# Kernel tuning notes

Hardware: AMD Instinct MI355X
Metric: run time of the kernel (lower is better)

## Reference

```python
import jax, jax.numpy as jnp
import numpy as np

EMBED = 1024
HEADS = 16
HEAD_DIM = EMBED // HEADS
MLP_DIM = 4096
EPS = 1e-5


def setup_inputs() -> dict:
    key = jax.random.key(0)
    ks = jax.random.split(key, 12)
    s = lambda d: 1.0 / np.sqrt(d)
    return {
        "x": jax.random.normal(ks[0], (8, 1024, EMBED), dtype=jnp.float32),
        "ln1_g": jnp.ones((EMBED,), jnp.float32),
        "ln1_b": jnp.zeros((EMBED,), jnp.float32),
        "w_qkv": jax.random.normal(ks[1], (EMBED, 3 * EMBED), jnp.float32) * s(EMBED),
        "b_qkv": jnp.zeros((3 * EMBED,), jnp.float32),
        "w_proj": jax.random.normal(ks[2], (EMBED, EMBED), jnp.float32) * s(EMBED),
        "b_proj": jnp.zeros((EMBED,), jnp.float32),
        "ln2_g": jnp.ones((EMBED,), jnp.float32),
        "ln2_b": jnp.zeros((EMBED,), jnp.float32),
        "w_fc1": jax.random.normal(ks[3], (EMBED, MLP_DIM), jnp.float32) * s(EMBED),
        "b_fc1": jnp.zeros((MLP_DIM,), jnp.float32),
        "w_fc2": jax.random.normal(ks[4], (MLP_DIM, EMBED), jnp.float32) * s(MLP_DIM),
        "b_fc2": jnp.zeros((EMBED,), jnp.float32),
    }


def _layernorm(x, g, b):
    mu = jnp.mean(x, axis=-1, keepdims=True)
    var = jnp.mean(jnp.square(x - mu), axis=-1, keepdims=True)
    return (x - mu) * jax.lax.rsqrt(var + EPS) * g + b


def reference(x, ln1_g, ln1_b, w_qkv, b_qkv, w_proj, b_proj,
              ln2_g, ln2_b, w_fc1, b_fc1, w_fc2, b_fc2):
    B, N, D = x.shape
    scale = HEAD_DIM ** -0.5

    # --- attention branch ---
    h = _layernorm(x, ln1_g, ln1_b)
    qkv = h @ w_qkv + b_qkv                       # [B,N,3D]
    qkv = qkv.reshape(B, N, 3, HEADS, HEAD_DIM)
    q, k, v = jnp.moveaxis(qkv, 2, 0)             # each [B,N,H,hd]
    attn = jnp.einsum('bqhd,bkhd->bhqk', q, k) * scale
    attn = jax.nn.softmax(attn, axis=-1)
    out = jnp.einsum('bhqk,bkhd->bqhd', attn, v).reshape(B, N, D)
    x = x + (out @ w_proj + b_proj)

    # --- MLP branch ---
    h = _layernorm(x, ln2_g, ln2_b)
    h = jax.nn.gelu(h @ w_fc1 + b_fc1, approximate=False)
    x = x + (h @ w_fc2 + b_fc2)
    return x
```

## Files before the change

kernel.cpp:

```cpp
#include <hip/hip_runtime.h>
#include <cstdint>


typedef unsigned short u16;
typedef short short8 __attribute__((ext_vector_type(8)));
typedef float floatx4 __attribute__((ext_vector_type(4)));

#define GLB(p) ((const __attribute__((address_space(1))) void*)(p))
#define LDSP(p) ((__attribute__((address_space(3))) void*)(p))

__device__ __forceinline__ u16 f2bf(float f) {
    uint32_t u = __float_as_uint(f);
    u += 0x7fffu + ((u >> 16) & 1u);
    return (u16)(u >> 16);
}
__device__ __forceinline__ uint32_t pack2(float a, float b) {
    return (uint32_t)f2bf(a) | ((uint32_t)f2bf(b) << 16);
}
__device__ __forceinline__ float fast_gelu(float v) {
    float u = v * (0.7978845608f + 0.0356774081f * v * v);
    float e = __expf(2.0f * u);
    float th = 1.0f - 2.0f * __builtin_amdgcn_rcpf(e + 1.0f);
    return 0.5f * v * (1.0f + th);
}

__global__ __launch_bounds__(256) void transpose_cast_kernel(
    const float* __restrict__ W, u16* __restrict__ Wt, int K, int N)
{
    __shared__ float tile[32][33];
    int n0 = blockIdx.x * 32, k0 = blockIdx.y * 32;
    int tx = threadIdx.x, ty = threadIdx.y;
    #pragma unroll
    for (int i = 0; i < 4; ++i)
        tile[ty + i * 8][tx] = W[(size_t)(k0 + ty + i * 8) * N + n0 + tx];
    __syncthreads();
    #pragma unroll
    for (int i = 0; i < 4; ++i)
        Wt[(size_t)(n0 + ty + i * 8) * K + k0 + tx] = f2bf(tile[tx][ty + i * 8]);
}

__global__ __launch_bounds__(256) void ln_kernel(
    const float* __restrict__ x, const float* __restrict__ gw,
    const float* __restrict__ bw, u16* __restrict__ out)
{
    const int row = blockIdx.x, tid = threadIdx.x;
    float4 v = ((const float4*)(x + (size_t)row * 1024))[tid];
    float s  = v.x + v.y + v.z + v.w;
    float ss = v.x * v.x + v.y * v.y + v.z * v.z + v.w * v.w;
    #pragma unroll
    for (int off = 32; off > 0; off >>= 1) {
        s  += __shfl_down(s, off);
        ss += __shfl_down(ss, off);
    }
    __shared__ float red[8];
    if ((tid & 63) == 0) { red[tid >> 6] = s; red[4 + (tid >> 6)] = ss; }
    __syncthreads();
    float S  = red[0] + red[1] + red[2] + red[3];
    float SS = red[4] + red[5] + red[6] + red[7];
    float mu  = S * (1.0f / 1024.0f);
    float var = SS * (1.0f / 1024.0f) - mu * mu;
    float rs  = rsqrtf(var + 1e-5f);
    float4 g4 = ((const float4*)gw)[tid];
    float4 b4 = ((const float4*)bw)[tid];
    u16* o = out + (size_t)row * 1024 + tid * 4;
    o[0] = f2bf((v.x - mu) * rs * g4.x + b4.x);
    o[1] = f2bf((v.y - mu) * rs * g4.y + b4.y);
    o[2] = f2bf((v.z - mu) * rs * g4.z + b4.z);
    o[3] = f2bf((v.w - mu) * rs * g4.w + b4.w);
}

#define MODE_BF16      0
#define MODE_BF16_GELU 1
#define MODE_F32_RES   2
#define MODE_QKV       3

template<int MODE>
__global__ __launch_bounds__(256) void gemm_bt_kernel(
    const u16* __restrict__ A, const u16* __restrict__ Bt,
    const float* __restrict__ bias, const float* __restrict__ res,
    void* __restrict__ outv, u16* __restrict__ vt, int M, int N, int K)
{
    __shared__ __attribute__((aligned(16))) u16 As[128 * 64];
    __shared__ __attribute__((aligned(16))) u16 Bs[128 * 64];
    const int tid = threadIdx.x;
    const int wave = tid >> 6, lane = tid & 63;
    const int lg = lane >> 4, lc = lane & 15;
    const int m0 = blockIdx.y * 128, n0 = blockIdx.x * 128;
    const int wr = wave >> 1, wc = wave & 1;

    floatx4 acc[4][4];
    #pragma unroll
    for (int i = 0; i < 4; ++i)
        #pragma unroll
        for (int j = 0; j < 4; ++j) acc[i][j] = floatx4{0.f, 0.f, 0.f, 0.f};

    const int srow = lane >> 3;
    const int schunk = (lane & 7) ^ srow;
    const u16* Ag = A  + (size_t)(m0 + wave * 32 + srow) * K + schunk * 8;
    const u16* Bg = Bt + (size_t)(n0 + wave * 32 + srow) * K + schunk * 8;
    u16* Asw = &As[wave * 4 * 512];
    u16* Bsw = &Bs[wave * 4 * 512];

    const int kiters = K >> 6;
    for (int kt = 0; kt < kiters; ++kt) {
        #pragma unroll
        for (int j = 0; j < 4; ++j) {
            __builtin_amdgcn_global_load_lds(GLB(Ag + (size_t)j * 8 * K), LDSP(Asw + j * 512), 16, 0, 0);
            __builtin_amdgcn_global_load_lds(GLB(Bg + (size_t)j * 8 * K), LDSP(Bsw + j * 512), 16, 0, 0);
        }
        Ag += 64; Bg += 64;
        __syncthreads();
        #pragma unroll
        for (int ks = 0; ks < 2; ++ks) {
            short8 fa[4], fb[4];
            #pragma unroll
            for (int mt = 0; mt < 4; ++mt)
                fa[mt] = *(const short8*)&As[(wr * 64 + mt * 16 + lc) * 64 +
                                             (((ks * 4 + lg) ^ (lc & 7)) * 8)];
            #pragma unroll
            for (int nt = 0; nt < 4; ++nt)
                fb[nt] = *(const short8*)&Bs[(wc * 64 + nt * 16 + lc) * 64 +
                                             (((ks * 4 + lg) ^ (lc & 7)) * 8)];
            #pragma unroll
            for (int mt = 0; mt < 4; ++mt)
                #pragma unroll
                for (int nt = 0; nt < 4; ++nt)
                    acc[mt][nt] = __builtin_amdgcn_mfma_f32_16x16x32_bf16(fa[mt], fb[nt], acc[mt][nt], 0, 0, 0);
        }
        __syncthreads();
    }

    if (MODE == MODE_QKV && n0 >= 2048) {
        #pragma unroll
        for (int mt = 0; mt < 4; ++mt) {
            #pragma unroll
            for (int nt = 0; nt < 4; ++nt) {
                const int col = n0 + wc * 64 + nt * 16 + lc;
                const float bv = bias[col];
                const int hd = col - 2048;
                const int rowbase = m0 + wr * 64 + mt * 16 + lg * 4;
                const int b = rowbase >> 10, token = rowbase & 1023;
                float v0 = acc[mt][nt][0] + bv, v1 = acc[mt][nt][1] + bv;
                float v2 = acc[mt][nt][2] + bv, v3 = acc[mt][nt][3] + bv;
                uint2 pk = {pack2(v0, v1), pack2(v2, v3)};
                *(uint2*)&vt[((size_t)b * 1024 + hd) * 1024 + token] = pk;
            }
        }
        return;
    }
    #pragma unroll
    for (int mt = 0; mt < 4; ++mt) {
        #pragma unroll
        for (int nt = 0; nt < 4; ++nt) {
            const int col = n0 + wc * 64 + nt * 16 + lc;
            const float bv = bias[col];
            #pragma unroll
            for (int r = 0; r < 4; ++r) {
                const int row = m0 + wr * 64 + mt * 16 + lg * 4 + r;
                float v = acc[mt][nt][r] + bv;
                if (MODE == MODE_BF16 || MODE == MODE_QKV) {
                    ((u16*)outv)[(size_t)row * N + col] = f2bf(v);
                } else if (MODE == MODE_BF16_GELU) {
                    ((u16*)outv)[(size_t)row * N + col] = f2bf(fast_gelu(v));
                } else {
                    ((float*)outv)[(size_t)row * N + col] = v + res[(size_t)row * N + col];
                }
            }
        }
    }
}

__global__ __launch_bounds__(256) void attn_kernel(
    const u16* __restrict__ qkv, const u16* __restrict__ vtg, u16* __restrict__ out)
{
    const int bid = blockIdx.x;
    const int g = ((bid >> 7) << 3) | (bid & 7);
    const int qt = (bid >> 3) & 15;
    const int h = g & 15, b = g >> 4;
    const int tid = threadIdx.x, wave = tid >> 6, lane = tid & 63;
    const int lg = lane >> 4, lc = lane & 15;

    __shared__ __attribute__((aligned(16))) u16 Qs[64 * 64];
    __shared__ __attribute__((aligned(16))) u16 Ks[64 * 64];
    __shared__ __attribute__((aligned(16))) u16 Vts[64 * 64];
    __shared__ __attribute__((aligned(16))) u16 Ps[64 * 64];

    const int q0 = qt * 64;
    const size_t hb = ((size_t)b * 1024) * 3072 + h * 64;
    const u16* vhead = vtg + ((size_t)b * 1024 + h * 64) * 1024;
    const int srow = lane >> 3;
    const int schunk = (lane & 7) ^ srow;

    {
        const u16* Qg = qkv + hb + (size_t)(q0 + wave * 16 + srow) * 3072 + schunk * 8;
        u16* Qw = &Qs[wave * 1024];
        __builtin_amdgcn_global_load_lds(GLB(Qg), LDSP(Qw), 16, 0, 0);
        __builtin_amdgcn_global_load_lds(GLB(Qg + (size_t)8 * 3072), LDSP(Qw + 512), 16, 0, 0);
    }
    __syncthreads();
    short8 aq[2];
    aq[0] = *(const short8*)&Qs[(wave * 16 + lc) * 64 + (((0 + lg) ^ (lc & 7)) * 8)];
    aq[1] = *(const short8*)&Qs[(wave * 16 + lc) * 64 + (((4 + lg) ^ (lc & 7)) * 8)];

    floatx4 o[4];
    #pragma unroll
    for (int dt = 0; dt < 4; ++dt) o[dt] = floatx4{0.f, 0.f, 0.f, 0.f};
    float mprev = -INFINITY, lsum = 0.f;
    const float sc = 0.125f;

    for (int kt = 0; kt < 16; ++kt) {
        __syncthreads();
        {
            const u16* Kg = qkv + hb + 1024 +
                (size_t)(kt * 64 + wave * 16 + srow) * 3072 + schunk * 8;
            u16* Kw = &Ks[wave * 1024];
            __builtin_amdgcn_global_load_lds(GLB(Kg), LDSP(Kw), 16, 0, 0);
            __builtin_amdgcn_global_load_lds(GLB(Kg + (size_t)8 * 3072), LDSP(Kw + 512), 16, 0, 0);
        }
        {
            const u16* Vg = vhead + (size_t)(wave * 16 + srow) * 1024 + kt * 64 + schunk * 8;
            u16* Vw = &Vts[wave * 1024];
            __builtin_amdgcn_global_load_lds(GLB(Vg), LDSP(Vw), 16, 0, 0);
            __builtin_amdgcn_global_load_lds(GLB(Vg + (size_t)8 * 1024), LDSP(Vw + 512), 16, 0, 0);
        }
        __syncthreads();

        floatx4 st[4];
        #pragma unroll
        for (int nt = 0; nt < 4; ++nt) st[nt] = floatx4{0.f, 0.f, 0.f, 0.f};
        #pragma unroll
        for (int ks = 0; ks < 2; ++ks)
            #pragma unroll
            for (int nt = 0; nt < 4; ++nt) {
                short8 fk = *(const short8*)&Ks[(nt * 16 + lc) * 64 +
                                                (((ks * 4 + lg) ^ (lc & 7)) * 8)];
                st[nt] = __builtin_amdgcn_mfma_f32_16x16x32_bf16(fk, aq[ks], st[nt], 0, 0, 0);
            }

        float m = st[0][0];
        #pragma unroll
        for (int nt = 0; nt < 4; ++nt)
            #pragma unroll
            for (int r = 0; r < 4; ++r) m = fmaxf(m, st[nt][r]);
        m = fmaxf(m, __shfl_xor(m, 16));
        m = fmaxf(m, __shfl_xor(m, 32));
        float mn = fmaxf(mprev, m * sc);
        float aexp = __expf(mprev - mn);
        mprev = mn;

        const int q = wave * 16 + lc;
        float rs = 0.f;
        #pragma unroll
        for (int nt = 0; nt < 4; ++nt) {
            float p0 = __expf(st[nt][0] * sc - mn);
            float p1 = __expf(st[nt][1] * sc - mn);
            float p2 = __expf(st[nt][2] * sc - mn);
            float p3 = __expf(st[nt][3] * sc - mn);
            rs += (p0 + p1) + (p2 + p3);
            const int c16 = nt * 2 + (lg >> 1);
            uint2 pk = {pack2(p0, p1), pack2(p2, p3)};
            *(uint2*)&Ps[q * 64 + ((c16 ^ (lc & 7)) * 8) + (lg & 1) * 4] = pk;
        }
        rs += __shfl_xor(rs, 16);
        rs += __shfl_xor(rs, 32);
        lsum = lsum * aexp + rs;
        #pragma unroll
        for (int dt = 0; dt < 4; ++dt)
            #pragma unroll
            for (int r = 0; r < 4; ++r) o[dt][r] *= aexp;

        #pragma unroll
        for (int ks = 0; ks < 2; ++ks) {
            short8 fp = *(const short8*)&Ps[q * 64 + (((ks * 4 + lg) ^ (lc & 7)) * 8)];
            #pragma unroll
            for (int dt = 0; dt < 4; ++dt) {
                short8 fv = *(const short8*)&Vts[(dt * 16 + lc) * 64 +
                                                 (((ks * 4 + lg) ^ (lc & 7)) * 8)];
                o[dt] = __builtin_amdgcn_mfma_f32_16x16x32_bf16(fv, fp, o[dt], 0, 0, 0);
            }
        }
    }

    const float rl = 1.0f / lsum;
    const int q = q0 + wave * 16 + lc;
    #pragma unroll
    for (int dt = 0; dt < 4; ++dt) {
        uint2 pk = {pack2(o[dt][0] * rl, o[dt][1] * rl),
                    pack2(o[dt][2] * rl, o[dt][3] * rl)};
        *(uint2*)&out[((size_t)b * 1024 + q) * 1024 + h * 64 + dt * 16 + lg * 4] = pk;
    }
}

extern "C" void kernel_launch(void* const* d_in, const int* in_sizes, int n_in,
                              void* d_out, int out_size, void* d_ws, size_t ws_size,
                              hipStream_t stream)
{
    const float* x      = (const float*)d_in[0];
    const float* ln1_g  = (const float*)d_in[1];
    const float* ln1_b  = (const float*)d_in[2];
    const float* w_qkv  = (const float*)d_in[3];
    const float* b_qkv  = (const float*)d_in[4];
    const float* w_proj = (const float*)d_in[5];
    const float* b_proj = (const float*)d_in[6];
    const float* ln2_g  = (const float*)d_in[7];
    const float* ln2_b  = (const float*)d_in[8];
    const float* w_fc1  = (const float*)d_in[9];
    const float* b_fc1  = (const float*)d_in[10];
    const float* w_fc2  = (const float*)d_in[11];
    const float* b_fc2  = (const float*)d_in[12];
    float* outp = (float*)d_out;

    char* ws = (char*)d_ws;
    size_t off = 0;
    auto alloc = [&](size_t bytes) { void* p = ws + off; off += (bytes + 255) & ~(size_t)255; return p; };
    u16*  wqkvT  = (u16*)alloc((size_t)3072 * 1024 * 2);
    u16*  wprojT = (u16*)alloc((size_t)1024 * 1024 * 2);
    u16*  wfc1T  = (u16*)alloc((size_t)4096 * 1024 * 2);
    u16*  wfc2T  = (u16*)alloc((size_t)1024 * 4096 * 2);
    u16*  hbuf   = (u16*)alloc((size_t)8192 * 1024 * 2);
    u16*  big    = (u16*)alloc((size_t)8192 * 4096 * 2);
    u16*  vtbuf  = (u16*)alloc((size_t)8 * 1024 * 1024 * 2);
    u16*  attno  = (u16*)alloc((size_t)8192 * 1024 * 2);
    float* x2    = (float*)alloc((size_t)8192 * 1024 * 4);

    dim3 tb(32, 8);
    transpose_cast_kernel<<<dim3(3072 / 32, 1024 / 32), tb, 0, stream>>>(w_qkv,  wqkvT,  1024, 3072);
    transpose_cast_kernel<<<dim3(1024 / 32, 1024 / 32), tb, 0, stream>>>(w_proj, wprojT, 1024, 1024);
    transpose_cast_kernel<<<dim3(4096 / 32, 1024 / 32), tb, 0, stream>>>(w_fc1,  wfc1T,  1024, 4096);
    transpose_cast_kernel<<<dim3(1024 / 32, 4096 / 32), tb, 0, stream>>>(w_fc2,  wfc2T,  4096, 1024);

    ln_kernel<<<8192, 256, 0, stream>>>(x, ln1_g, ln1_b, hbuf);
    gemm_bt_kernel<MODE_QKV><<<dim3(3072 / 128, 8192 / 128), 256, 0, stream>>>(
        hbuf, wqkvT, b_qkv, nullptr, big, vtbuf, 8192, 3072, 1024);
    attn_kernel<<<2048, 256, 0, stream>>>(big, vtbuf, attno);
    gemm_bt_kernel<MODE_F32_RES><<<dim3(1024 / 128, 8192 / 128), 256, 0, stream>>>(
        attno, wprojT, b_proj, x, x2, nullptr, 8192, 1024, 1024);
    ln_kernel<<<8192, 256, 0, stream>>>(x2, ln2_g, ln2_b, hbuf);
    gemm_bt_kernel<MODE_BF16_GELU><<<dim3(4096 / 128, 8192 / 128), 256, 0, stream>>>(
        hbuf, wfc1T, b_fc1, nullptr, big, nullptr, 8192, 4096, 1024);
    gemm_bt_kernel<MODE_F32_RES><<<dim3(1024 / 128, 8192 / 128), 256, 0, stream>>>(
        big, wfc2T, b_fc2, x2, outp, nullptr, 8192, 1024, 4096);
}
```

Baseline: 517.8 us.

## Triple-buffer GEMM LDS with async prefetch and 256x128 tiles

Replaces the single-buffered 128x128 GEMM with a 512-thread kernel that computes 256x128 tiles. It keeps three dynamic-LDS stages and prefetches two K-tiles ahead with global_load_lds, waiting on vmcnt instead of double __syncthreads. MFMA blocks are wrapped in s_setprio to favour matrix issue. The aim is to hide global-load latency and raise arithmetic intensity per block, at the cost of 144KB of LDS per block, which limits each CU to one block, plus redundant loads of the last tile at the tail.

```diff
diff --git a/kernel.cpp b/kernel.cpp
--- a/kernel.cpp
+++ b/kernel.cpp
@@ -74,18 +74,20 @@
 #define MODE_F32_RES   2
 #define MODE_QKV       3
 
+#define G3_BUFSZ 24576
+#define G3_LDS_BYTES 147456
+
 template<int MODE>
-__global__ __launch_bounds__(256) void gemm_bt_kernel(
+__global__ __launch_bounds__(512, 2) void gemm3_kernel(
     const u16* __restrict__ A, const u16* __restrict__ Bt,
     const float* __restrict__ bias, const float* __restrict__ res,
     void* __restrict__ outv, u16* __restrict__ vt, int M, int N, int K)
 {
-    __shared__ __attribute__((aligned(16))) u16 As[128 * 64];
-    __shared__ __attribute__((aligned(16))) u16 Bs[128 * 64];
+    extern __shared__ u16 lds[];
     const int tid = threadIdx.x;
     const int wave = tid >> 6, lane = tid & 63;
     const int lg = lane >> 4, lc = lane & 15;
-    const int m0 = blockIdx.y * 128, n0 = blockIdx.x * 128;
+    const int m0 = blockIdx.y * 256, n0 = blockIdx.x * 128;
     const int wr = wave >> 1, wc = wave & 1;
 
     floatx4 acc[4][4];
@@ -96,52 +98,81 @@
 
     const int srow = lane >> 3;
     const int schunk = (lane & 7) ^ srow;
-    const u16* Ag = A  + (size_t)(m0 + wave * 32 + srow) * K + schunk * 8;
-    const u16* Bg = Bt + (size_t)(n0 + wave * 32 + srow) * K + schunk * 8;
-    u16* Asw = &As[wave * 4 * 512];
-    u16* Bsw = &Bs[wave * 4 * 512];
-
-    const int kiters = K >> 6;
-    for (int kt = 0; kt < kiters; ++kt) {
-        #pragma unroll
-        for (int j = 0; j < 4; ++j) {
-            __builtin_amdgcn_global_load_lds(GLB(Ag + (size_t)j * 8 * K), LDSP(Asw + j * 512), 16, 0, 0);
-            __builtin_amdgcn_global_load_lds(GLB(Bg + (size_t)j * 8 * K), LDSP(Bsw + j * 512), 16, 0, 0);
-        }
-        Ag += 64; Bg += 64;
-        __syncthreads();
+
+    const u16* gsrc[6];
+    int ldsoff[6];
+    #pragma unroll
+    for (int j = 0; j < 6; ++j) {
+        const int g = wave * 6 + j;
+        if (g < 32) {
+            gsrc[j]   = A  + (size_t)(m0 + g * 8 + srow) * K + schunk * 8;
+            ldsoff[j] = g * 512;
+        } else {
+            gsrc[j]   = Bt + (size_t)(n0 + (g - 32) * 8 + srow) * K + schunk * 8;
+            ldsoff[j] = 16384 + (g - 32) * 512;
+        }
+    }
+
+    const int nt = K >> 6;
+    auto stage = [&](int b, int kk) {
+        u16* base = lds + b * G3_BUFSZ;
+        #pragma unroll
+        for (int j = 0; j < 6; ++j)
+            __builtin_amdgcn_global_load_lds(GLB(gsrc[j] + kk), LDSP(base + ldsoff[j]), 16, 0, 0);
+    };
+
+    stage(0, 0);
+    stage(1, 64);
+    asm volatile("s_waitcnt vmcnt(6)" ::: "memory");
+    __builtin_amdgcn_s_barrier();
+    __builtin_amdgcn_sched_barrier(0);
+
+    int cur = 0;
+    for (int t = 0; t < nt; ++t) {
+        const int tn = t + 2;
+        const int kk = (tn < nt ? tn : nt - 1) << 6;
+        const int nb = (cur >= 1) ? cur - 1 : cur + 2;
+        stage(nb, kk);
+
+        const u16* Ab = lds + cur * G3_BUFSZ;
+        const u16* Bb = Ab + 16384;
         #pragma unroll
         for (int ks = 0; ks < 2; ++ks) {
             short8 fa[4], fb[4];
             #pragma unroll
             for (int mt = 0; mt < 4; ++mt)
-                fa[mt] = *(const short8*)&As[(wr * 64 + mt * 16 + lc) * 64 +
+                fa[mt] = *(const short8*)&Ab[(wr * 64 + mt * 16 + lc) * 64 +
                                              (((ks * 4 + lg) ^ (lc & 7)) * 8)];
             #pragma unroll
-            for (int nt = 0; nt < 4; ++nt)
-                fb[nt] = *(const short8*)&Bs[(wc * 64 + nt * 16 + lc) * 64 +
+            for (int nn = 0; nn < 4; ++nn)
+                fb[nn] = *(const short8*)&Bb[(wc * 64 + nn * 16 + lc) * 64 +
                                              (((ks * 4 + lg) ^ (lc & 7)) * 8)];
+            __builtin_amdgcn_s_setprio(1);
             #pragma unroll
             for (int mt = 0; mt < 4; ++mt)
                 #pragma unroll
-                for (int nt = 0; nt < 4; ++nt)
-                    acc[mt][nt] = __builtin_amdgcn_mfma_f32_16x16x32_bf16(fa[mt], fb[nt], acc[mt][nt], 0, 0, 0);
-        }
-        __syncthreads();
+                for (int nn = 0; nn < 4; ++nn)
+                    acc[mt][nn] = __builtin_amdgcn_mfma_f32_16x16x32_bf16(fa[mt], fb[nn], acc[mt][nn], 0, 0, 0);
+            __builtin_amdgcn_s_setprio(0);
+        }
+        asm volatile("s_waitcnt vmcnt(6)" ::: "memory");
+        __builtin_amdgcn_s_barrier();
+        __builtin_amdgcn_sched_barrier(0);
+        cur = (cur + 1 == 3) ? 0 : cur + 1;
     }
 
     if (MODE == MODE_QKV && n0 >= 2048) {
         #pragma unroll
         for (int mt = 0; mt < 4; ++mt) {
             #pragma unroll
-            for (int nt = 0; nt < 4; ++nt) {
-                const int col = n0 + wc * 64 + nt * 16 + lc;
+            for (int nn = 0; nn < 4; ++nn) {
+                const int col = n0 + wc * 64 + nn * 16 + lc;
                 const float bv = bias[col];
                 const int hd = col - 2048;
                 const int rowbase = m0 + wr * 64 + mt * 16 + lg * 4;
                 const int b = rowbase >> 10, token = rowbase & 1023;
-                float v0 = acc[mt][nt][0] + bv, v1 = acc[mt][nt][1] + bv;
-                float v2 = acc[mt][nt][2] + bv, v3 = acc[mt][nt][3] + bv;
+                float v0 = acc[mt][nn][0] + bv, v1 = acc[mt][nn][1] + bv;
+                float v2 = acc[mt][nn][2] + bv, v3 = acc[mt][nn][3] + bv;
                 uint2 pk = {pack2(v0, v1), pack2(v2, v3)};
                 *(uint2*)&vt[((size_t)b * 1024 + hd) * 1024 + token] = pk;
             }
@@ -151,13 +182,13 @@
     #pragma unroll
     for (int mt = 0; mt < 4; ++mt) {
         #pragma unroll
-        for (int nt = 0; nt < 4; ++nt) {
-            const int col = n0 + wc * 64 + nt * 16 + lc;
+        for (int nn = 0; nn < 4; ++nn) {
+            const int col = n0 + wc * 64 + nn * 16 + lc;
             const float bv = bias[col];
             #pragma unroll
             for (int r = 0; r < 4; ++r) {
                 const int row = m0 + wr * 64 + mt * 16 + lg * 4 + r;
-                float v = acc[mt][nt][r] + bv;
+                float v = acc[mt][nn][r] + bv;
                 if (MODE == MODE_BF16 || MODE == MODE_QKV) {
                     ((u16*)outv)[(size_t)row * N + col] = f2bf(v);
                 } else if (MODE == MODE_BF16_GELU) {
@@ -323,6 +354,17 @@
     u16*  attno  = (u16*)alloc((size_t)8192 * 1024 * 2);
     float* x2    = (float*)alloc((size_t)8192 * 1024 * 4);
 
+    static bool attr_done = []{
+        hipFuncSetAttribute(reinterpret_cast<const void*>(gemm3_kernel<MODE_QKV>),
+                            hipFuncAttributeMaxDynamicSharedMemorySize, G3_LDS_BYTES);
+        hipFuncSetAttribute(reinterpret_cast<const void*>(gemm3_kernel<MODE_BF16_GELU>),
+                            hipFuncAttributeMaxDynamicSharedMemorySize, G3_LDS_BYTES);
+        hipFuncSetAttribute(reinterpret_cast<const void*>(gemm3_kernel<MODE_F32_RES>),
+                            hipFuncAttributeMaxDynamicSharedMemorySize, G3_LDS_BYTES);
+        return true;
+    }();
+    (void)attr_done;
+
     dim3 tb(32, 8);
     transpose_cast_kernel<<<dim3(3072 / 32, 1024 / 32), tb, 0, stream>>>(w_qkv,  wqkvT,  1024, 3072);
     transpose_cast_kernel<<<dim3(1024 / 32, 1024 / 32), tb, 0, stream>>>(w_proj, wprojT, 1024, 1024);
@@ -330,14 +372,14 @@
     transpose_cast_kernel<<<dim3(1024 / 32, 4096 / 32), tb, 0, stream>>>(w_fc2,  wfc2T,  4096, 1024);
 
     ln_kernel<<<8192, 256, 0, stream>>>(x, ln1_g, ln1_b, hbuf);
-    gemm_bt_kernel<MODE_QKV><<<dim3(3072 / 128, 8192 / 128), 256, 0, stream>>>(
+    gemm3_kernel<MODE_QKV><<<dim3(3072 / 128, 8192 / 256), 512, G3_LDS_BYTES, stream>>>(
         hbuf, wqkvT, b_qkv, nullptr, big, vtbuf, 8192, 3072, 1024);
     attn_kernel<<<2048, 256, 0, stream>>>(big, vtbuf, attno);
-    gemm_bt_kernel<MODE_F32_RES><<<dim3(1024 / 128, 8192 / 128), 256, 0, stream>>>(
+    gemm3_kernel<MODE_F32_RES><<<dim3(1024 / 128, 8192 / 256), 512, G3_LDS_BYTES, stream>>>(
         attno, wprojT, b_proj, x, x2, nullptr, 8192, 1024, 1024);
     ln_kernel<<<8192, 256, 0, stream>>>(x2, ln2_g, ln2_b, hbuf);
-    gemm_bt_kernel<MODE_BF16_GELU><<<dim3(4096 / 128, 8192 / 128), 256, 0, stream>>>(
+    gemm3_kernel<MODE_BF16_GELU><<<dim3(4096 / 128, 8192 / 256), 512, G3_LDS_BYTES, stream>>>(
         hbuf, wfc1T, b_fc1, nullptr, big, nullptr, 8192, 4096, 1024);
-    gemm_bt_kernel<MODE_F32_RES><<<dim3(1024 / 128, 8192 / 128), 256, 0, stream>>>(
+    gemm3_kernel<MODE_F32_RES><<<dim3(1024 / 128, 8192 / 256), 512, G3_LDS_BYTES, stream>>>(
         big, wfc2T, b_fc2, x2, outp, nullptr, 8192, 1024, 4096);
 }
```

After: 513.4 us. No clear change (-0.9%).
